# Kernel optimization log

Hardware: AMD Instinct MI355X
Metric: run time of the kernel (lower is better)

## Reference

```python
import jax, jax.numpy as jnp
import numpy as np

N_HEAD = 16
COND_LEN = 256  # n_unmasked; mask[i, j] == 1 iff j < COND_LEN + i


def rotate_half(x):
    # interleaved pairs: (x0, x1, x2, x3, ...) -> (-x1, x0, -x3, x2, ...)
    x = x.reshape(x.shape[:-1] + (-1, 2))
    x1, x2 = x[..., 0], x[..., 1]
    return jnp.stack([-x2, x1], axis=-1).reshape(x.shape[:-2] + (-1,))


def apply_rotary_pos_emb(t, freqs):
    # t: [B, H, T, l], freqs: [T, l] -> broadcast over B, H
    return t * jnp.cos(freqs) + rotate_half(t) * jnp.sin(freqs)


def setup_inputs() -> dict:
    key = jax.random.key(0)
    ks = jax.random.split(key, 12)
    B, T, C = 8, 769, 1024
    l = 32
    s = 0.02
    return {
        "x_q": jax.random.normal(ks[0], (B, T, C), jnp.float32),
        "x_kv": jax.random.normal(ks[1], (B, T, C), jnp.float32),
        "rotary_pos_emb": jax.random.uniform(ks[2], (T, l), jnp.float32),
        "Wq": jax.random.normal(ks[3], (C, C), jnp.float32) * s,
        "bq": jnp.zeros((C,), jnp.float32),
        "Wk": jax.random.normal(ks[4], (C, C), jnp.float32) * s,
        "bk": jnp.zeros((C,), jnp.float32),
        "Wv": jax.random.normal(ks[5], (C, C), jnp.float32) * s,
        "bv": jnp.zeros((C,), jnp.float32),
        "Wp": jax.random.normal(ks[6], (C, C), jnp.float32) * s,
        "bp": jnp.zeros((C,), jnp.float32),
    }


def reference(x_q, x_kv, rotary_pos_emb, Wq, bq, Wk, bk, Wv, bv, Wp, bp):
    B, T_q, C = x_q.shape
    T_kv = x_kv.shape[1]
    H = N_HEAD
    hd = C // H

    def heads(x, W, b, T):
        return (x @ W.T + b).reshape(B, T, H, hd).transpose(0, 2, 1, 3)  # [B,H,T,hd]

    q = heads(x_q, Wq, bq, T_q)
    k = heads(x_kv, Wk, bk, T_kv)
    v = heads(x_kv, Wv, bv, T_kv)

    # partial rotary on first l dims of q and k
    l = rotary_pos_emb.shape[-1]
    q = jnp.concatenate([apply_rotary_pos_emb(q[..., :l], rotary_pos_emb), q[..., l:]], axis=-1)
    k = jnp.concatenate([apply_rotary_pos_emb(k[..., :l], rotary_pos_emb), k[..., l:]], axis=-1)

    att = jnp.einsum("bhqd,bhkd->bhqk", q, k) * (1.0 / jnp.sqrt(jnp.asarray(hd, q.dtype)))
    # custom prefix+causal mask: allowed iff col < COND_LEN + row
    row = jnp.arange(T_q)[:, None]
    col = jnp.arange(T_kv)[None, :]
    allowed = col < (COND_LEN + row)  # [T_q, T_kv]
    att = jnp.where(allowed[None, None], att, -jnp.inf)
    att = jax.nn.softmax(att, axis=-1)

    y = jnp.einsum("bhqk,bhkd->bhqd", att, v)
    y = y.transpose(0, 2, 1, 3).reshape(B, T_q, C)
    return y @ Wp.T + bp
```

## Files before the change

### kernel.cpp

```cpp
#include <hip/hip_runtime.h>
#include <stdint.h>

#define B_    8
#define T_    769
#define C_    1024
#define H_    16
#define COND_ 256
#define NTOK  (B_*T_)
#define BH_   (B_*H_)

typedef short    v8s  __attribute__((ext_vector_type(8)));
typedef float    v4f  __attribute__((ext_vector_type(4)));
typedef uint16_t u16x4 __attribute__((ext_vector_type(4)));
typedef uint16_t u16x8 __attribute__((ext_vector_type(8)));

__device__ __forceinline__ uint16_t f2bf(float f) {
  uint32_t u = __builtin_bit_cast(uint32_t, f);
  u += 0x7fffu + ((u >> 16) & 1u);
  return (uint16_t)(u >> 16);
}
__device__ __forceinline__ float bf2f(uint16_t h) {
  uint32_t u = ((uint32_t)h) << 16;
  return __builtin_bit_cast(float, u);
}

__device__ __forceinline__ void gl_lds16(const void* gptr, void* lptr) {
  __builtin_amdgcn_global_load_lds(
      (const __attribute__((address_space(1))) uint32_t*)gptr,
      (__attribute__((address_space(3))) uint32_t*)lptr,
      16, 0, 0);
}

__global__ __launch_bounds__(256) void convert_bf16(
    const float* xq, const float* xkv, const float* wq, const float* wk,
    const float* wv, const float* wp,
    uint16_t* dxq, uint16_t* dxkv, uint16_t* dwq, uint16_t* dwk,
    uint16_t* dwv, uint16_t* dwp)
{
  int bid = blockIdx.x;
  const float* s; uint16_t* d; int base;
  if (bid < 6152)       { s = xq;  d = dxq;  base = bid; }
  else if (bid < 12304) { s = xkv; d = dxkv; base = bid - 6152; }
  else {
    int r = bid - 12304;
    int wsel = r >> 10; base = r & 1023;
    s = (wsel == 0) ? wq : (wsel == 1) ? wk : (wsel == 2) ? wv : wp;
    d = (wsel == 0) ? dwq : (wsel == 1) ? dwk : (wsel == 2) ? dwv : dwp;
  }
  int i = base * 256 + threadIdx.x;
  float4 f = ((const float4*)s)[i];
  u16x4 o;
  o[0] = f2bf(f.x); o[1] = f2bf(f.y); o[2] = f2bf(f.z); o[3] = f2bf(f.w);
  ((u16x4*)d)[i] = o;
}

__device__ __forceinline__ void gemm_tile_mainloop(
    const uint16_t* A, const uint16_t* W, int M, int row0, int col0,
    v4f acc[4][4], uint16_t* sA, uint16_t* sB)
{
  const int tid = threadIdx.x;
  const int lane = tid & 63, w = tid >> 6, quad = lane >> 4, l15 = lane & 15;
  const int rbase = (w >> 1) * 64, cbase = (w & 1) * 64;

  const int c0 = tid, c1 = tid + 256;
  const int am0 = c0 >> 2, am1 = c1 >> 2;
  const int aq0 = (c0 & 3) * 8, aq1 = (c1 & 3) * 8;
  const uint16_t* Ar0 = A + (size_t)min(row0 + am0, M - 1) * 1024 + aq0;
  const uint16_t* Ar1 = A + (size_t)min(row0 + am1, M - 1) * 1024 + aq1;
  const uint16_t* Br0 = W + (size_t)(col0 + am0) * 1024 + aq0;
  const uint16_t* Br1 = W + (size_t)(col0 + am1) * 1024 + aq1;

  #pragma unroll
  for (int i = 0; i < 4; i++)
    #pragma unroll
    for (int j = 0; j < 4; j++) acc[i][j] = (v4f)0.0f;

  for (int k0 = 0; k0 < 1024; k0 += 32) {
    gl_lds16(Ar0 + k0, sA + c0 * 8);
    gl_lds16(Ar1 + k0, sA + c1 * 8);
    gl_lds16(Br0 + k0, sB + c0 * 8);
    gl_lds16(Br1 + k0, sB + c1 * 8);
    __syncthreads();
    v8s af[4], bf[4];
    #pragma unroll
    for (int i = 0; i < 4; i++) {
      int m = rbase + i * 16 + l15;
      af[i] = *(const v8s*)(sA + m * 32 + quad * 8);
    }
    #pragma unroll
    for (int j = 0; j < 4; j++) {
      int n = cbase + j * 16 + l15;
      bf[j] = *(const v8s*)(sB + n * 32 + quad * 8);
    }
    #pragma unroll
    for (int i = 0; i < 4; i++)
      #pragma unroll
      for (int j = 0; j < 4; j++)
        acc[i][j] = __builtin_amdgcn_mfma_f32_16x16x32_bf16(af[i], bf[j], acc[i][j], 0, 0, 0);
    __syncthreads();
  }
}

__global__ __launch_bounds__(256) void gemm_qkv(
    const uint16_t* xq, const uint16_t* xkv,
    const uint16_t* wq, const uint16_t* wk, const uint16_t* wv,
    const float* bq, const float* bk, const float* bv, const float* freqs,
    uint16_t* Q, uint16_t* K, uint16_t* V)
{
  __shared__ uint16_t sA[128 * 32];
  __shared__ uint16_t sB[128 * 32];
  const int z = blockIdx.z;
  const uint16_t* A = (z == 0) ? xq : xkv;
  const uint16_t* W = (z == 0) ? wq : (z == 1 ? wk : wv);
  const float* bias  = (z == 0) ? bq : (z == 1 ? bk : bv);
  uint16_t* dst      = (z == 0) ? Q  : (z == 1 ? K  : V);
  const int row0 = blockIdx.x * 128, col0 = blockIdx.y * 128;

  v4f acc[4][4];
  gemm_tile_mainloop(A, W, NTOK, row0, col0, acc, sA, sB);

  const int tid = threadIdx.x;
  const int lane = tid & 63, w = tid >> 6, quad = lane >> 4, l15 = lane & 15;
  const int rbase = (w >> 1) * 64, cbase = (w & 1) * 64;
  #pragma unroll
  for (int i = 0; i < 4; i++) {
    #pragma unroll
    for (int reg = 0; reg < 4; reg++) {
      int n = row0 + rbase + i * 16 + quad * 4 + reg;
      bool ok = (n < NTOK);
      int nn = min(n, NTOK - 1);
      int b = nn / T_, t = nn % T_;
      float vj[4];
      #pragma unroll
      for (int j = 0; j < 4; j++)
        vj[j] = acc[i][j][reg] + bias[col0 + cbase + j * 16 + l15];
      if (z < 2) {
        float v0 = vj[0], v1 = vj[1];
        float p0 = __shfl_xor(v0, 1);
        float p1 = __shfl_xor(v1, 1);
        float f0 = freqs[t * 32 + l15];
        float f1 = freqs[t * 32 + 16 + l15];
        float s0, c0, s1, c1;
        __sincosf(f0, &s0, &c0);
        __sincosf(f1, &s1, &c1);
        if (l15 & 1) { vj[0] = v0 * c0 + p0 * s0; vj[1] = v1 * c1 + p1 * s1; }
        else         { vj[0] = v0 * c0 - p0 * s0; vj[1] = v1 * c1 - p1 * s1; }
      }
      if (z == 0) {
        #pragma unroll
        for (int j = 0; j < 4; j++) vj[j] *= 0.125f;
      }
      if (ok) {
        #pragma unroll
        for (int j = 0; j < 4; j++) {
          int col = col0 + cbase + j * 16 + l15;
          int h = col >> 6, d = col & 63;
          dst[((size_t)(b * H_ + h) * T_ + t) * 64 + d] = f2bf(vj[j]);
        }
      }
    }
  }
}

__global__ __launch_bounds__(256) void gemm_out(
    const uint16_t* Y, const uint16_t* wp, const float* bp, float* out)
{
  __shared__ uint16_t sA[128 * 32];
  __shared__ uint16_t sB[128 * 32];
  const int row0 = blockIdx.x * 128, col0 = blockIdx.y * 128;
  v4f acc[4][4];
  gemm_tile_mainloop(Y, wp, NTOK, row0, col0, acc, sA, sB);

  const int tid = threadIdx.x;
  const int lane = tid & 63, w = tid >> 6, quad = lane >> 4, l15 = lane & 15;
  const int rbase = (w >> 1) * 64, cbase = (w & 1) * 64;
  #pragma unroll
  for (int i = 0; i < 4; i++) {
    #pragma unroll
    for (int reg = 0; reg < 4; reg++) {
      int n = row0 + rbase + i * 16 + quad * 4 + reg;
      if (n < NTOK) {
        #pragma unroll
        for (int j = 0; j < 4; j++) {
          int col = col0 + cbase + j * 16 + l15;
          out[(size_t)n * 1024 + col] = acc[i][j][reg] + bp[col];
        }
      }
    }
  }
}

__global__ __launch_bounds__(256) void attn(
    const uint16_t* Q, const uint16_t* K, const uint16_t* V, uint16_t* Y)
{
  __shared__ uint16_t sK[128 * 64];
  __shared__ uint16_t sVT[64 * 136];
  __shared__ uint16_t sP[4 * 16 * 136];

  const int tid = threadIdx.x;
  const int lane = tid & 63, w = tid >> 6, quad = lane >> 4, l15 = lane & 15;
  const int bh = blockIdx.y, b = bh >> 4, h = bh & 15;
  const int q0 = blockIdx.x * 64;

  const uint16_t* Qb = Q + (size_t)bh * T_ * 64;
  const uint16_t* Kb = K + (size_t)bh * T_ * 64;
  const uint16_t* Vb = V + (size_t)bh * T_ * 64;

  const int qr = min(q0 + w * 16 + l15, T_ - 1);
  v8s aq0 = *(const v8s*)(Qb + (size_t)qr * 64 + quad * 8);
  v8s aq1 = *(const v8s*)(Qb + (size_t)qr * 64 + 32 + quad * 8);

  float l_r[4] = {0.f, 0.f, 0.f, 0.f};
  v4f o[4];
  #pragma unroll
  for (int r = 0; r < 4; r++) o[r] = (v4f)0.0f;

  const int kend = min(T_, q0 + 319);
  const int nkt = (kend + 127) >> 7;

  for (int kt = 0; kt < nkt; kt++) {
    const int k0 = kt * 128;
    #pragma unroll
    for (int r = 0; r < 4; r++) {
      int c = r * 256 + tid;
      int key = c >> 3, qp = c & 7;
      int g = qp ^ (key & 7);
      int gk = min(k0 + key, T_ - 1);
      gl_lds16(Kb + (size_t)gk * 64 + g * 8, sK + c * 8);
    }
    #pragma unroll
    for (int hv = 0; hv < 2; hv++) {
      #pragma unroll
      for (int r = 0; r < 2; r++) {
        int d0 = (r * 4 + w) * 8;
        int kl = hv * 64 + lane;
        int gk = min(k0 + kl, T_ - 1);
        u16x8 vv = *(const u16x8*)(Vb + (size_t)gk * 64 + d0);
        #pragma unroll
        for (int j = 0; j < 8; j++) sVT[(d0 + j) * 136 + kl] = vv[j];
      }
    }
    __syncthreads();

    v4f s[8];
    #pragma unroll
    for (int cb = 0; cb < 8; cb++) {
      int key_l = cb * 16 + l15;
      v8s b0 = *(const v8s*)(sK + (key_l * 8 + ((quad) ^ (key_l & 7))) * 8);
      v8s b1 = *(const v8s*)(sK + (key_l * 8 + ((4 + quad) ^ (key_l & 7))) * 8);
      v4f zz = (v4f)0.0f;
      zz = __builtin_amdgcn_mfma_f32_16x16x32_bf16(aq0, b0, zz, 0, 0, 0);
      zz = __builtin_amdgcn_mfma_f32_16x16x32_bf16(aq1, b1, zz, 0, 0, 0);
      s[cb] = zz;
    }

    uint16_t* pw = sP + w * (16 * 136);
    const int qrow_base = q0 + w * 16 + quad * 4;
    const bool full = (k0 + 128 <= COND_ + q0) && (k0 + 128 <= T_);
    if (full) {
      #pragma unroll
      for (int reg = 0; reg < 4; reg++) {
        float rs = 0.f;
        #pragma unroll
        for (int cb = 0; cb < 8; cb++) {
          float pv = __expf(s[cb][reg]);
          uint16_t pb = f2bf(pv);
          rs += bf2f(pb);
          pw[(quad * 4 + reg) * 136 + cb * 16 + l15] = pb;
        }
        #pragma unroll
        for (int off = 1; off < 16; off <<= 1) rs += __shfl_xor(rs, off);
        l_r[reg] += rs;
      }
    } else {
      #pragma unroll
      for (int reg = 0; reg < 4; reg++) {
        int lim = min(COND_ + qrow_base + reg, T_);
        float rs = 0.f;
        #pragma unroll
        for (int cb = 0; cb < 8; cb++) {
          int key = k0 + cb * 16 + l15;
          float pv = (key < lim) ? __expf(s[cb][reg]) : 0.f;
          uint16_t pb = f2bf(pv);
          rs += bf2f(pb);
          pw[(quad * 4 + reg) * 136 + cb * 16 + l15] = pb;
        }
        #pragma unroll
        for (int off = 1; off < 16; off <<= 1) rs += __shfl_xor(rs, off);
        l_r[reg] += rs;
      }
    }

    #pragma unroll
    for (int ks = 0; ks < 4; ks++) {
      v8s ap = *(const v8s*)(pw + l15 * 136 + ks * 32 + quad * 8);
      #pragma unroll
      for (int cbd = 0; cbd < 4; cbd++) {
        v8s bv = *(const v8s*)(sVT + (cbd * 16 + l15) * 136 + ks * 32 + quad * 8);
        o[cbd] = __builtin_amdgcn_mfma_f32_16x16x32_bf16(ap, bv, o[cbd], 0, 0, 0);
      }
    }
    __syncthreads();
  }

  #pragma unroll
  for (int reg = 0; reg < 4; reg++) {
    int t = q0 + w * 16 + quad * 4 + reg;
    if (t < T_) {
      float inv = 1.0f / l_r[reg];
      #pragma unroll
      for (int cbd = 0; cbd < 4; cbd++) {
        int d = cbd * 16 + l15;
        Y[((size_t)(b * T_ + t)) * C_ + h * 64 + d] = f2bf(o[cbd][reg] * inv);
      }
    }
  }
}

extern "C" void kernel_launch(void* const* d_in, const int* in_sizes, int n_in,
                              void* d_out, int out_size, void* d_ws, size_t ws_size,
                              hipStream_t stream)
{
  const float* x_q   = (const float*)d_in[0];
  const float* x_kv  = (const float*)d_in[1];
  const float* freqs = (const float*)d_in[2];
  const float* Wq = (const float*)d_in[3];
  const float* bq = (const float*)d_in[4];
  const float* Wk = (const float*)d_in[5];
  const float* bk = (const float*)d_in[6];
  const float* Wv = (const float*)d_in[7];
  const float* bv = (const float*)d_in[8];
  const float* Wp = (const float*)d_in[9];
  const float* bp = (const float*)d_in[10];
  float* out = (float*)d_out;

  const size_t SZX = (size_t)NTOK * C_;
  const size_t SZW = (size_t)C_ * C_;
  uint16_t* ws = (uint16_t*)d_ws;
  uint16_t* xq_bf  = ws;
  uint16_t* xkv_bf = xq_bf + SZX;
  uint16_t* wq_bf  = xkv_bf + SZX;
  uint16_t* wk_bf  = wq_bf + SZW;
  uint16_t* wv_bf  = wk_bf + SZW;
  uint16_t* wp_bf  = wv_bf + SZW;
  uint16_t* Qb = wp_bf + SZW;
  uint16_t* Kb = Qb + SZX;
  uint16_t* Vb = Kb + SZX;
  uint16_t* Yb = Vb + SZX;

  convert_bf16<<<dim3(16400), 256, 0, stream>>>(
      x_q, x_kv, Wq, Wk, Wv, Wp, xq_bf, xkv_bf, wq_bf, wk_bf, wv_bf, wp_bf);

  gemm_qkv<<<dim3(49, 8, 3), 256, 0, stream>>>(
      xq_bf, xkv_bf, wq_bf, wk_bf, wv_bf, bq, bk, bv, freqs, Qb, Kb, Vb);

  attn<<<dim3(13, BH_), 256, 0, stream>>>(Qb, Kb, Vb, Yb);

  gemm_out<<<dim3(49, 8), 256, 0, stream>>>(Yb, wp_bf, bp, out);
}
```

Before: 287.8 us.

## Use BK=64 XOR-swizzled LDS tiles and column-major block order in GEMMs

The GEMM main loop now stages 64-wide K slices instead of 32, which halves the number of barrier pairs per tile. The LDS layout is XOR-swizzled to avoid bank conflicts on the MFMA operand reads. The QKV launch becomes a 2D grid that indexes the contiguous Wq/Wk/Wv buffers as one concatenated weight, with column tiles on the fastest grid axis so blocks sharing an activation row tile run together. LDS use per block doubles, which may lower occupancy.

```diff
diff --git a/kernel.cpp b/kernel.cpp
--- a/kernel.cpp
+++ b/kernel.cpp
@@ -54,7 +54,7 @@
   ((u16x4*)d)[i] = o;
 }
 
-__device__ __forceinline__ void gemm_tile_mainloop(
+__device__ __forceinline__ void gemm_mainloop64(
     const uint16_t* A, const uint16_t* W, int M, int row0, int col0,
     v4f acc[4][4], uint16_t* sA, uint16_t* sB)
 {
@@ -62,62 +62,68 @@
   const int lane = tid & 63, w = tid >> 6, quad = lane >> 4, l15 = lane & 15;
   const int rbase = (w >> 1) * 64, cbase = (w & 1) * 64;
 
-  const int c0 = tid, c1 = tid + 256;
-  const int am0 = c0 >> 2, am1 = c1 >> 2;
-  const int aq0 = (c0 & 3) * 8, aq1 = (c1 & 3) * 8;
-  const uint16_t* Ar0 = A + (size_t)min(row0 + am0, M - 1) * 1024 + aq0;
-  const uint16_t* Ar1 = A + (size_t)min(row0 + am1, M - 1) * 1024 + aq1;
-  const uint16_t* Br0 = W + (size_t)(col0 + am0) * 1024 + aq0;
-  const uint16_t* Br1 = W + (size_t)(col0 + am1) * 1024 + aq1;
+  const uint16_t* Aptr[4];
+  const uint16_t* Bptr[4];
+  #pragma unroll
+  for (int r = 0; r < 4; r++) {
+    int c = r * 256 + tid;
+    int row = c >> 3, qp = c & 7;
+    int g = qp ^ (row & 7);
+    Aptr[r] = A + (size_t)min(row0 + row, M - 1) * 1024 + g * 8;
+    Bptr[r] = W + (size_t)(col0 + row) * 1024 + g * 8;
+  }
 
   #pragma unroll
   for (int i = 0; i < 4; i++)
     #pragma unroll
     for (int j = 0; j < 4; j++) acc[i][j] = (v4f)0.0f;
 
-  for (int k0 = 0; k0 < 1024; k0 += 32) {
-    gl_lds16(Ar0 + k0, sA + c0 * 8);
-    gl_lds16(Ar1 + k0, sA + c1 * 8);
-    gl_lds16(Br0 + k0, sB + c0 * 8);
-    gl_lds16(Br1 + k0, sB + c1 * 8);
+  for (int k0 = 0; k0 < 1024; k0 += 64) {
+    #pragma unroll
+    for (int r = 0; r < 4; r++) {
+      gl_lds16(Aptr[r] + k0, sA + (r * 256 + tid) * 8);
+      gl_lds16(Bptr[r] + k0, sB + (r * 256 + tid) * 8);
+    }
     __syncthreads();
-    v8s af[4], bf[4];
-    #pragma unroll
-    for (int i = 0; i < 4; i++) {
-      int m = rbase + i * 16 + l15;
-      af[i] = *(const v8s*)(sA + m * 32 + quad * 8);
-    }
-    #pragma unroll
-    for (int j = 0; j < 4; j++) {
-      int n = cbase + j * 16 + l15;
-      bf[j] = *(const v8s*)(sB + n * 32 + quad * 8);
-    }
-    #pragma unroll
-    for (int i = 0; i < 4; i++)
-      #pragma unroll
-      for (int j = 0; j < 4; j++)
-        acc[i][j] = __builtin_amdgcn_mfma_f32_16x16x32_bf16(af[i], bf[j], acc[i][j], 0, 0, 0);
+    #pragma unroll
+    for (int s = 0; s < 2; s++) {
+      v8s af[4], bf[4];
+      #pragma unroll
+      for (int i = 0; i < 4; i++) {
+        int m = rbase + i * 16 + l15;
+        af[i] = *(const v8s*)(sA + m * 64 + (((s * 4 + quad) ^ (m & 7)) * 8));
+      }
+      #pragma unroll
+      for (int j = 0; j < 4; j++) {
+        int n = cbase + j * 16 + l15;
+        bf[j] = *(const v8s*)(sB + n * 64 + (((s * 4 + quad) ^ (n & 7)) * 8));
+      }
+      #pragma unroll
+      for (int i = 0; i < 4; i++)
+        #pragma unroll
+        for (int j = 0; j < 4; j++)
+          acc[i][j] = __builtin_amdgcn_mfma_f32_16x16x32_bf16(af[i], bf[j], acc[i][j], 0, 0, 0);
+    }
     __syncthreads();
   }
 }
 
 __global__ __launch_bounds__(256) void gemm_qkv(
-    const uint16_t* xq, const uint16_t* xkv,
-    const uint16_t* wq, const uint16_t* wk, const uint16_t* wv,
+    const uint16_t* xq, const uint16_t* xkv, const uint16_t* Wqkv,
     const float* bq, const float* bk, const float* bv, const float* freqs,
     uint16_t* Q, uint16_t* K, uint16_t* V)
 {
-  __shared__ uint16_t sA[128 * 32];
-  __shared__ uint16_t sB[128 * 32];
-  const int z = blockIdx.z;
+  __shared__ uint16_t sA[128 * 64];
+  __shared__ uint16_t sB[128 * 64];
+  const int ct = blockIdx.x, rt = blockIdx.y;
+  const int z = ct >> 3;
+  const int col0 = ct * 128, row0 = rt * 128;
   const uint16_t* A = (z == 0) ? xq : xkv;
-  const uint16_t* W = (z == 0) ? wq : (z == 1 ? wk : wv);
   const float* bias  = (z == 0) ? bq : (z == 1 ? bk : bv);
   uint16_t* dst      = (z == 0) ? Q  : (z == 1 ? K  : V);
-  const int row0 = blockIdx.x * 128, col0 = blockIdx.y * 128;
 
   v4f acc[4][4];
-  gemm_tile_mainloop(A, W, NTOK, row0, col0, acc, sA, sB);
+  gemm_mainloop64(A, Wqkv, NTOK, row0, col0, acc, sA, sB);
 
   const int tid = threadIdx.x;
   const int lane = tid & 63, w = tid >> 6, quad = lane >> 4, l15 = lane & 15;
@@ -133,7 +139,7 @@
       float vj[4];
       #pragma unroll
       for (int j = 0; j < 4; j++)
-        vj[j] = acc[i][j][reg] + bias[col0 + cbase + j * 16 + l15];
+        vj[j] = acc[i][j][reg] + bias[(col0 + cbase + j * 16 + l15) & 1023];
       if (z < 2) {
         float v0 = vj[0], v1 = vj[1];
         float p0 = __shfl_xor(v0, 1);
@@ -154,7 +160,7 @@
         #pragma unroll
         for (int j = 0; j < 4; j++) {
           int col = col0 + cbase + j * 16 + l15;
-          int h = col >> 6, d = col & 63;
+          int h = (col >> 6) & 15, d = col & 63;
           dst[((size_t)(b * H_ + h) * T_ + t) * 64 + d] = f2bf(vj[j]);
         }
       }
@@ -165,11 +171,11 @@
 __global__ __launch_bounds__(256) void gemm_out(
     const uint16_t* Y, const uint16_t* wp, const float* bp, float* out)
 {
-  __shared__ uint16_t sA[128 * 32];
-  __shared__ uint16_t sB[128 * 32];
-  const int row0 = blockIdx.x * 128, col0 = blockIdx.y * 128;
+  __shared__ uint16_t sA[128 * 64];
+  __shared__ uint16_t sB[128 * 64];
+  const int col0 = blockIdx.x * 128, row0 = blockIdx.y * 128;
   v4f acc[4][4];
-  gemm_tile_mainloop(Y, wp, NTOK, row0, col0, acc, sA, sB);
+  gemm_mainloop64(Y, wp, NTOK, row0, col0, acc, sA, sB);
 
   const int tid = threadIdx.x;
   const int lane = tid & 63, w = tid >> 6, quad = lane >> 4, l15 = lane & 15;
@@ -351,10 +357,10 @@
   convert_bf16<<<dim3(16400), 256, 0, stream>>>(
       x_q, x_kv, Wq, Wk, Wv, Wp, xq_bf, xkv_bf, wq_bf, wk_bf, wv_bf, wp_bf);
 
-  gemm_qkv<<<dim3(49, 8, 3), 256, 0, stream>>>(
-      xq_bf, xkv_bf, wq_bf, wk_bf, wv_bf, bq, bk, bv, freqs, Qb, Kb, Vb);
+  gemm_qkv<<<dim3(24, 49), 256, 0, stream>>>(
+      xq_bf, xkv_bf, wq_bf, bq, bk, bv, freqs, Qb, Kb, Vb);
 
   attn<<<dim3(13, BH_), 256, 0, stream>>>(Qb, Kb, Vb, Yb);
 
-  gemm_out<<<dim3(49, 8), 256, 0, stream>>>(Yb, wp_bf, bp, out);
-}
+  gemm_out<<<dim3(8, 49), 256, 0, stream>>>(Yb, wp_bf, bp, out);
+}
```

Result: faster. 280.9 us (-2.4%).
